# Kernel tuning notes

Hardware: AMD Instinct MI355X
Metric: run time of the kernel (lower is better)

## Reference

```python
import jax, jax.numpy as jnp
import numpy as np

N = 50000
E_RAND = 800000
F_IN = 128
HID = 128
HEADS = 8
LAYERS = 2
DH = HID // HEADS  # 16


def setup_inputs() -> dict:
    key = jax.random.key(0)
    ks = jax.random.split(key, 8)
    x = jax.random.normal(ks[0], (N, F_IN), dtype=jnp.float32)
    # random edges + self loops so every row of the segment-softmax is nonempty
    rnd = jax.random.randint(ks[1], (2, E_RAND), 0, N, dtype=jnp.int32)
    loops = jnp.tile(jnp.arange(N, dtype=jnp.int32), (2, 1))
    edge_idx = jnp.concatenate([rnd, loops], axis=1)  # [2, 850000]
    edge_vals = jnp.ones((edge_idx.shape[1],), dtype=jnp.float32)
    # glorot-style params
    enc_W = jax.random.normal(ks[2], (F_IN, HID), dtype=jnp.float32) * np.sqrt(2.0 / (F_IN + HID))
    enc_b = jnp.zeros((HID,), dtype=jnp.float32)
    W_stack = jax.random.normal(ks[3], (LAYERS, HEADS, HID, DH), dtype=jnp.float32) * np.sqrt(2.0 / (HID + DH))
    a_stack = jax.random.normal(ks[4], (LAYERS, HEADS, 2 * DH), dtype=jnp.float32) * np.sqrt(2.0 / (1 + 2 * DH))
    return {"x": x, "edge_idx": edge_idx, "edge_vals": edge_vals,
            "enc_W": enc_W, "enc_b": enc_b, "W_stack": W_stack, "a_stack": a_stack}


def _gat_layer(xin, row, col, edge_vals, W, a):
    # xin: [N, HID]; W: [H, HID, DH]; a: [H, 2*DH]
    n = xin.shape[0]
    h = jnp.einsum('nd,hdf->hnf', xin, W)            # [H, N, DH]
    a_src, a_dst = a[:, :DH], a[:, DH:]
    alpha_src = jnp.einsum('hnf,hf->hn', h, a_src)   # a . h[row] part
    alpha_dst = jnp.einsum('hnf,hf->hn', h, a_dst)   # a . h[col] part
    logits = edge_vals[None, :] * (alpha_src[:, row] + alpha_dst[:, col])  # [H, E]
    e = jnp.exp(jax.nn.leaky_relu(logits, 0.2))      # unnormalized attention
    rowsum = jax.ops.segment_sum(e.T, row, num_segments=n)               # [N, H]
    msg = e[:, :, None] * h[:, col, :]               # [H, E, DH]
    agg = jax.vmap(lambda m: jax.ops.segment_sum(m, row, num_segments=n))(msg)  # [H, N, DH]
    out = agg / rowsum.T[:, :, None]
    return jnp.transpose(out, (1, 0, 2)).reshape(n, -1)  # concat heads -> [N, HID]


def reference(x, edge_idx, edge_vals, enc_W, enc_b, W_stack, a_stack):
    row, col = edge_idx[0], edge_idx[1]
    xc = x @ enc_W + enc_b  # encoder
    L = W_stack.shape[0]
    for ell in range(L):
        out = _gat_layer(xc, row, col, edge_vals, W_stack[ell], a_stack[ell])
        if ell != L - 1:
            out = jax.nn.elu(out)  # feat_drop is identity in eval mode
        xc = out + xc if ell > 0 else out  # use_residual=True
    # single snapshot: stack over T=1 then permute(1,0,2) -> [N, 1, HID]
    return xc[:, None, :]
```

## Files before the change

kernel.cpp:

```cpp
#include <hip/hip_runtime.h>
#include <hip/hip_bf16.h>


typedef __attribute__((ext_vector_type(8))) short short8;
typedef __attribute__((ext_vector_type(4))) float floatx4;
typedef __attribute__((ext_vector_type(2))) float floatx2;

__device__ __forceinline__ unsigned f2u(float f) { return __float_as_uint(f); }
__device__ __forceinline__ float u2f(unsigned u) { return __uint_as_float(u); }
__device__ __forceinline__ unsigned short f2bf_rne(float x) {
    unsigned u = f2u(x);
    unsigned r = (u + 0x7FFF + ((u >> 16) & 1)) >> 16;
    return (unsigned short)r;
}
__device__ __forceinline__ float bf2f(unsigned short b) { return u2f(((unsigned)b) << 16); }


__global__ void histpack_kernel(const int* __restrict__ row, int* __restrict__ deg,
                                int* __restrict__ rank, int E, int EB,
                                const float* __restrict__ encW,
                                const float* __restrict__ Wstack,
                                short8* __restrict__ Wh, short8* __restrict__ Wl) {
    int b = blockIdx.x;
    if (b < EB) {
        int e = b * 256 + threadIdx.x;
        if (e < E) rank[e] = atomicAdd(&deg[row[e]], 1);
        return;
    }
    int idx = (b - EB) * 256 + threadIdx.x;
    if (idx >= 3 * 2048) return;
    int mat = idx >> 11;
    int r = idx & 2047;
    int lane = r & 63;
    int tile = r >> 6;
    int ct = tile >> 2, kt = tile & 3;
    int ncol = ct * 16 + (lane & 15);
    int k0 = kt * 32 + ((lane >> 4) * 8);
    short8 hv, lv;
#pragma unroll
    for (int j = 0; j < 8; ++j) {
        int k = k0 + j;
        float w = (mat == 0)
            ? encW[k * 128 + ncol]
            : Wstack[(mat - 1) * 16384 + (ncol >> 4) * 2048 + k * 16 + (ncol & 15)];
        unsigned u = f2u(w);
        hv[j] = (short)(u >> 16);
        float hf = u2f(u & 0xFFFF0000u);
        float l = w - hf;
        lv[j] = (short)(f2u(l) >> 16);
    }
    Wh[idx] = hv;
    Wl[idx] = lv;
}

__global__ void scan_atomic_kernel(const int* __restrict__ deg, int* __restrict__ rowstart,
                                   int* __restrict__ gcursor, int n) {
    __shared__ int sd[512];
    __shared__ int sbase;
    int t = threadIdx.x;
    int idx = blockIdx.x * 512 + t;
    int v = (idx < n) ? deg[idx] : 0;
    sd[t] = v;
    __syncthreads();
    for (int off = 1; off < 512; off <<= 1) {
        int add = (t >= off) ? sd[t - off] : 0;
        __syncthreads();
        sd[t] += add;
        __syncthreads();
    }
    if (t == 511) sbase = atomicAdd(gcursor, sd[511]);
    __syncthreads();
    if (idx < n) rowstart[idx] = sbase + sd[t] - v;
}

__global__ void scatterperm_kernel(const int* __restrict__ row, const int* __restrict__ rank,
                                   const int* __restrict__ rowstart, int* __restrict__ perm,
                                   int E) {
    int e = blockIdx.x * 256 + threadIdx.x;
    if (e < E) perm[rowstart[row[e]] + rank[e]] = e;
}

__global__ void gathercv_kernel(const int* __restrict__ perm, const int* __restrict__ colv,
                                const float* __restrict__ ev, int2* __restrict__ csr_cv,
                                int E) {
    int s = blockIdx.x * 256 + threadIdx.x;
    if (s < E) {
        int e = perm[s];
        csr_cv[s] = make_int2(colv[e], __float_as_int(ev[e]));
    }
}


__global__ __launch_bounds__(256) void
gemm_mfma(const float* __restrict__ A, const short8* __restrict__ Bh,
          const short8* __restrict__ Bl, const float* __restrict__ bias,
          const float* __restrict__ avec, float* __restrict__ Cf,
          unsigned short* __restrict__ Cbf,
          float* __restrict__ asrc, float* __restrict__ adst, int n, int flags) {
    int wave = threadIdx.x >> 6;
    int lane = threadIdx.x & 63;
    int q = lane >> 4;
    int col = lane & 15;
    int n0w = blockIdx.x * 64 + wave * 16;

    int arow = min(n0w + col, n - 1);
    const float* Arow = A + (size_t)arow * 128;
    int kb = q * 8;
    short8 Ah[4], Al[4];
#pragma unroll
    for (int kt = 0; kt < 4; ++kt) {
        float4 f0 = *(const float4*)(Arow + kt * 32 + kb);
        float4 f1 = *(const float4*)(Arow + kt * 32 + kb + 4);
        float fv[8] = {f0.x, f0.y, f0.z, f0.w, f1.x, f1.y, f1.z, f1.w};
#pragma unroll
        for (int j = 0; j < 8; ++j) {
            unsigned u = f2u(fv[j]);
            Ah[kt][j] = (short)(u >> 16);
            float hf = u2f(u & 0xFFFF0000u);
            float l = fv[j] - hf;
            Al[kt][j] = (short)(f2u(l) >> 16);
        }
    }

    int nbase = n0w + q * 4;
#pragma unroll
    for (int ct = 0; ct < 8; ++ct) {
        short8 bh[4], bl[4];
#pragma unroll
        for (int kt = 0; kt < 4; ++kt) {
            bh[kt] = Bh[(ct * 4 + kt) * 64 + lane];
            bl[kt] = Bl[(ct * 4 + kt) * 64 + lane];
        }
        float bv = (flags & 1) ? bias[ct * 16 + col] : 0.f;
        floatx4 acc = {bv, bv, bv, bv};
#pragma unroll
        for (int kt = 0; kt < 4; ++kt) {
            acc = __builtin_amdgcn_mfma_f32_16x16x32_bf16(Ah[kt], bh[kt], acc, 0, 0, 0);
            acc = __builtin_amdgcn_mfma_f32_16x16x32_bf16(Al[kt], bh[kt], acc, 0, 0, 0);
            acc = __builtin_amdgcn_mfma_f32_16x16x32_bf16(Ah[kt], bl[kt], acc, 0, 0, 0);
        }
#pragma unroll
        for (int reg = 0; reg < 4; ++reg) {
            int node = nbase + reg;
            if (node < n) {
                if (flags & 4) Cbf[(size_t)node * 128 + ct * 16 + col] = f2bf_rne(acc[reg]);
                else           Cf[(size_t)node * 128 + ct * 16 + col] = acc[reg];
            }
        }
        if (flags & 2) {
            float a_s = avec[ct * 32 + col];
            float a_d = avec[ct * 32 + 16 + col];
#pragma unroll
            for (int reg = 0; reg < 4; ++reg) {
                float ps = acc[reg] * a_s;
                float pd = acc[reg] * a_d;
#pragma unroll
                for (int off = 8; off; off >>= 1) {
                    ps += __shfl_down(ps, off, 16);
                    pd += __shfl_down(pd, off, 16);
                }
                int node = nbase + reg;
                if (col == 0 && node < n) {
                    asrc[node * 8 + ct] = ps;
                    adst[node * 8 + ct] = pd;
                }
            }
        }
    }
}


#define PROC(W, JJ) if ((JJ) < e) {                                        \
    int c = (W).x;                                                          \
    float v = __int_as_float((W).y);                                        \
    float lg = v * (as_w + adst[c * 8 + h]);                                \
    float lr = fmaxf(lg, 0.2f * lg);                                        \
    float w = __expf(lr);                                                   \
    uint4 hv = *(const uint4*)(hbf + (size_t)c * 128 + l4 * 8);             \
    floatx2 wv = {w, w};                                                    \
    floatx2 p0 = {u2f(hv.x << 16), u2f(hv.x & 0xFFFF0000u)};                \
    floatx2 p1 = {u2f(hv.y << 16), u2f(hv.y & 0xFFFF0000u)};                \
    floatx2 p2 = {u2f(hv.z << 16), u2f(hv.z & 0xFFFF0000u)};                \
    floatx2 p3 = {u2f(hv.w << 16), u2f(hv.w & 0xFFFF0000u)};                \
    acc0 += wv * p0; acc1 += wv * p1; acc2 += wv * p2; acc3 += wv * p3;     \
    ws += w; }

__global__ __launch_bounds__(256) void
aggregate_kernel(const int* __restrict__ rowstart, const int* __restrict__ degv,
                 const int2* __restrict__ cv,
                 const unsigned short* __restrict__ hbf,
                 const float* __restrict__ asrc, const float* __restrict__ adst,
                 const float* __restrict__ resid, float* __restrict__ out,
                 int mode, int n) {
    int wid = (blockIdx.x * 256 + threadIdx.x) >> 6;
    if (wid >= n) return;
    int lane = threadIdx.x & 63;
    int grp = lane >> 4;
    int l4 = lane & 15;
    int h = l4 >> 1;

    int s = rowstart[wid];
    int e = s + degv[wid];
    float as_w = asrc[wid * 8 + h];

    floatx2 acc0 = {0.f, 0.f}, acc1 = {0.f, 0.f};
    floatx2 acc2 = {0.f, 0.f}, acc3 = {0.f, 0.f};
    float ws = 0.f;

    int jb = s + grp;
    int2 s0 = {0, 0}, s1 = {0, 0}, s2 = {0, 0}, s3 = {0, 0};
    if (jb      < e) s0 = cv[jb];
    if (jb + 4  < e) s1 = cv[jb + 4];
    if (jb + 8  < e) s2 = cv[jb + 8];
    if (jb + 12 < e) s3 = cv[jb + 12];

    while (jb < e) {
        int2 e0 = s0, e1 = s1, e2 = s2, e3 = s3;
        int jn = jb + 16;
        if (jn      < e) s0 = cv[jn];
        if (jn + 4  < e) s1 = cv[jn + 4];
        if (jn + 8  < e) s2 = cv[jn + 8];
        if (jn + 12 < e) s3 = cv[jn + 12];
        PROC(e0, jb)
        PROC(e1, jb + 4)
        PROC(e2, jb + 8)
        PROC(e3, jb + 12)
        jb = jn;
    }

    float a0 = acc0.x, a1 = acc0.y, a2 = acc1.x, a3 = acc1.y;
    float a4 = acc2.x, a5 = acc2.y, a6 = acc3.x, a7 = acc3.y;

#define RED4(x) x += __shfl_xor(x, 16); x += __shfl_xor(x, 32);
    RED4(a0) RED4(a1) RED4(a2) RED4(a3)
    RED4(a4) RED4(a5) RED4(a6) RED4(a7)
    RED4(ws)
#undef RED4

    if (grp == 0) {
        float inv = 1.0f / ws;
        float o[8] = {a0 * inv, a1 * inv, a2 * inv, a3 * inv,
                      a4 * inv, a5 * inv, a6 * inv, a7 * inv};
        size_t base = (size_t)wid * 128 + l4 * 8;
        if (mode == 0) {
#pragma unroll
            for (int k = 0; k < 8; ++k) o[k] = o[k] > 0.f ? o[k] : expm1f(o[k]);
        } else {
            float4 r0 = *(const float4*)(resid + base);
            float4 r1 = *(const float4*)(resid + base + 4);
            o[0] += r0.x; o[1] += r0.y; o[2] += r0.z; o[3] += r0.w;
            o[4] += r1.x; o[5] += r1.y; o[6] += r1.z; o[7] += r1.w;
        }
        float4 w0 = {o[0], o[1], o[2], o[3]};
        float4 w1 = {o[4], o[5], o[6], o[7]};
        *(float4*)(out + base) = w0;
        *(float4*)(out + base + 4) = w1;
    }
}
#undef PROC


extern "C" void kernel_launch(void* const* d_in, const int* in_sizes, int n_in,
                              void* d_out, int out_size, void* d_ws, size_t ws_size,
                              hipStream_t stream) {
    const int N = in_sizes[0] / 128;
    const int E = in_sizes[2];

    const float* x      = (const float*)d_in[0];
    const int*   eidx   = (const int*)d_in[1];
    const float* ev     = (const float*)d_in[2];
    const float* encW   = (const float*)d_in[3];
    const float* encb   = (const float*)d_in[4];
    const float* Wstack = (const float*)d_in[5];
    const float* astack = (const float*)d_in[6];
    float* out = (float*)d_out;

    const int* row = eidx;
    const int* colv = eidx + E;

    char* p = (char*)d_ws;
    float* xc   = (float*)p; p += (size_t)N * 128 * 4;
    float* xcB  = (float*)p; p += (size_t)N * 128 * 4;
    unsigned short* hbf = (unsigned short*)p; p += (size_t)N * 128 * 2;
    float* asrc = (float*)p; p += (size_t)N * 8 * 4;
    float* adst = (float*)p; p += (size_t)N * 8 * 4;
    short8* Wh  = (short8*)p; p += 3 * 2048 * 16;
    short8* Wl  = (short8*)p; p += 3 * 2048 * 16;
    int2* csr_cv = (int2*)p; p += (size_t)E * 8;
    int* rowstart = (int*)p; p += (size_t)N * 4;
    int* deg    = (int*)p;   p += (size_t)N * 4;
    int* gcursor = (int*)p;  p += 4;

    int* rank = (int*)xc;
    int* perm = rank + E;

    const int NB = (N + 511) / 512;
    const int GB = (N + 63) / 64;
    const int AGG = (N + 3) / 4;
    const int EB = (E + 255) / 256;

    hipMemsetAsync(deg, 0, (size_t)(N + 1) * 4, stream);
    histpack_kernel<<<EB + 24, 256, 0, stream>>>(row, deg, rank, E, EB,
                                                 encW, Wstack, Wh, Wl);
    scan_atomic_kernel<<<NB, 512, 0, stream>>>(deg, rowstart, gcursor, N);
    scatterperm_kernel<<<EB, 256, 0, stream>>>(row, rank, rowstart, perm, E);
    gathercv_kernel<<<EB, 256, 0, stream>>>(perm, colv, ev, csr_cv, E);

    gemm_mfma<<<GB, 256, 0, stream>>>(x, Wh, Wl, encb, nullptr, xc, nullptr,
                                      nullptr, nullptr, N, 1);

    gemm_mfma<<<GB, 256, 0, stream>>>(xc, Wh + 2048, Wl + 2048, nullptr, astack,
                                      nullptr, hbf, asrc, adst, N, 2 | 4);
    aggregate_kernel<<<AGG, 256, 0, stream>>>(rowstart, deg, csr_cv, hbf, asrc, adst,
                                              nullptr, xcB, 0, N);

    gemm_mfma<<<GB, 256, 0, stream>>>(xcB, Wh + 4096, Wl + 4096, nullptr, astack + 256,
                                      nullptr, hbf, asrc, adst, N, 2 | 4);
    aggregate_kernel<<<AGG, 256, 0, stream>>>(rowstart, deg, csr_cv, hbf, asrc, adst,
                                              xcB, out, 1, N);
}
```

Baseline: 317.4 us.

## Fuse encoder GEMM with degree scan and layer-1 GEMM with edge scatter

Merges independent work into shared launches. The encoder GEMM blocks and the row-offset scan blocks now run in one grid, and the layer-1 projection GEMM runs alongside the CSR permutation scatter. The rank/perm scratch moves from xc to xcB so the buffers do not collide. This cuts two kernel launches and lets the preprocessing overlap with the GEMMs. The aggregate loop's manual prefetch pipeline is also replaced by a simple unrolled loop, which may lower memory-level parallelism.

```diff
diff --git a/kernel.cpp b/kernel.cpp
--- a/kernel.cpp
+++ b/kernel.cpp
@@ -13,7 +13,6 @@
     unsigned r = (u + 0x7FFF + ((u >> 16) & 1)) >> 16;
     return (unsigned short)r;
 }
-__device__ __forceinline__ float bf2f(unsigned short b) { return u2f(((unsigned)b) << 16); }
 
 
 __global__ void histpack_kernel(const int* __restrict__ row, int* __restrict__ deg,
@@ -53,33 +52,6 @@
     Wl[idx] = lv;
 }
 
-__global__ void scan_atomic_kernel(const int* __restrict__ deg, int* __restrict__ rowstart,
-                                   int* __restrict__ gcursor, int n) {
-    __shared__ int sd[512];
-    __shared__ int sbase;
-    int t = threadIdx.x;
-    int idx = blockIdx.x * 512 + t;
-    int v = (idx < n) ? deg[idx] : 0;
-    sd[t] = v;
-    __syncthreads();
-    for (int off = 1; off < 512; off <<= 1) {
-        int add = (t >= off) ? sd[t - off] : 0;
-        __syncthreads();
-        sd[t] += add;
-        __syncthreads();
-    }
-    if (t == 511) sbase = atomicAdd(gcursor, sd[511]);
-    __syncthreads();
-    if (idx < n) rowstart[idx] = sbase + sd[t] - v;
-}
-
-__global__ void scatterperm_kernel(const int* __restrict__ row, const int* __restrict__ rank,
-                                   const int* __restrict__ rowstart, int* __restrict__ perm,
-                                   int E) {
-    int e = blockIdx.x * 256 + threadIdx.x;
-    if (e < E) perm[rowstart[row[e]] + rank[e]] = e;
-}
-
 __global__ void gathercv_kernel(const int* __restrict__ perm, const int* __restrict__ colv,
                                 const float* __restrict__ ev, int2* __restrict__ csr_cv,
                                 int E) {
@@ -91,8 +63,8 @@
 }
 
 
-__global__ __launch_bounds__(256) void
-gemm_mfma(const float* __restrict__ A, const short8* __restrict__ Bh,
+__device__ __forceinline__ void
+gemm_body(int bid, const float* __restrict__ A, const short8* __restrict__ Bh,
           const short8* __restrict__ Bl, const float* __restrict__ bias,
           const float* __restrict__ avec, float* __restrict__ Cf,
           unsigned short* __restrict__ Cbf,
@@ -101,7 +73,7 @@
     int lane = threadIdx.x & 63;
     int q = lane >> 4;
     int col = lane & 15;
-    int n0w = blockIdx.x * 64 + wave * 16;
+    int n0w = bid * 64 + wave * 16;
 
     int arow = min(n0w + col, n - 1);
     const float* Arow = A + (size_t)arow * 128;
@@ -169,21 +141,57 @@
     }
 }
 
-
-#define PROC(W, JJ) if ((JJ) < e) {                                        \
-    int c = (W).x;                                                          \
-    float v = __int_as_float((W).y);                                        \
-    float lg = v * (as_w + adst[c * 8 + h]);                                \
-    float lr = fmaxf(lg, 0.2f * lg);                                        \
-    float w = __expf(lr);                                                   \
-    uint4 hv = *(const uint4*)(hbf + (size_t)c * 128 + l4 * 8);             \
-    floatx2 wv = {w, w};                                                    \
-    floatx2 p0 = {u2f(hv.x << 16), u2f(hv.x & 0xFFFF0000u)};                \
-    floatx2 p1 = {u2f(hv.y << 16), u2f(hv.y & 0xFFFF0000u)};                \
-    floatx2 p2 = {u2f(hv.z << 16), u2f(hv.z & 0xFFFF0000u)};                \
-    floatx2 p3 = {u2f(hv.w << 16), u2f(hv.w & 0xFFFF0000u)};                \
-    acc0 += wv * p0; acc1 += wv * p1; acc2 += wv * p2; acc3 += wv * p3;     \
-    ws += w; }
+__global__ __launch_bounds__(256) void
+gemm_mfma(const float* __restrict__ A, const short8* __restrict__ Bh,
+          const short8* __restrict__ Bl, const float* __restrict__ avec,
+          unsigned short* __restrict__ Cbf,
+          float* __restrict__ asrc, float* __restrict__ adst, int n) {
+    gemm_body(blockIdx.x, A, Bh, Bl, nullptr, avec, nullptr, Cbf, asrc, adst, n, 2 | 4);
+}
+
+__global__ __launch_bounds__(256) void
+enc_scan_kernel(const float* __restrict__ x, const short8* __restrict__ Wh,
+                const short8* __restrict__ Wl, const float* __restrict__ encb,
+                float* __restrict__ xc, int n, int GBn,
+                const int* __restrict__ deg, int* __restrict__ rowstart,
+                int* __restrict__ gcursor) {
+    __shared__ int sd[256];
+    __shared__ int sbase;
+    if ((int)blockIdx.x < GBn) {
+        gemm_body(blockIdx.x, x, Wh, Wl, encb, nullptr, xc, nullptr, nullptr, nullptr, n, 1);
+        return;
+    }
+    int t = threadIdx.x;
+    int idx = (blockIdx.x - GBn) * 256 + t;
+    int v = (idx < n) ? deg[idx] : 0;
+    sd[t] = v;
+    __syncthreads();
+    for (int off = 1; off < 256; off <<= 1) {
+        int add = (t >= off) ? sd[t - off] : 0;
+        __syncthreads();
+        sd[t] += add;
+        __syncthreads();
+    }
+    if (t == 255) sbase = atomicAdd(gcursor, sd[255]);
+    __syncthreads();
+    if (idx < n) rowstart[idx] = sbase + sd[t] - v;
+}
+
+__global__ __launch_bounds__(256) void
+sperm_gemm_kernel(const float* __restrict__ xc, const short8* __restrict__ Wh1,
+                  const short8* __restrict__ Wl1, const float* __restrict__ avec,
+                  unsigned short* __restrict__ hbf, float* __restrict__ asrc,
+                  float* __restrict__ adst, int n, int GBn,
+                  const int* __restrict__ row, const int* __restrict__ rank,
+                  const int* __restrict__ rowstart, int* __restrict__ perm, int E) {
+    if ((int)blockIdx.x < GBn) {
+        gemm_body(blockIdx.x, xc, Wh1, Wl1, nullptr, avec, nullptr, hbf, asrc, adst, n, 2 | 4);
+        return;
+    }
+    int e = (blockIdx.x - GBn) * 256 + threadIdx.x;
+    if (e < E) perm[rowstart[row[e]] + rank[e]] = e;
+}
+
 
 __global__ __launch_bounds__(256) void
 aggregate_kernel(const int* __restrict__ rowstart, const int* __restrict__ degv,
@@ -207,25 +215,25 @@
     floatx2 acc2 = {0.f, 0.f}, acc3 = {0.f, 0.f};
     float ws = 0.f;
 
-    int jb = s + grp;
-    int2 s0 = {0, 0}, s1 = {0, 0}, s2 = {0, 0}, s3 = {0, 0};
-    if (jb      < e) s0 = cv[jb];
-    if (jb + 4  < e) s1 = cv[jb + 4];
-    if (jb + 8  < e) s2 = cv[jb + 8];
-    if (jb + 12 < e) s3 = cv[jb + 12];
-
-    while (jb < e) {
-        int2 e0 = s0, e1 = s1, e2 = s2, e3 = s3;
-        int jn = jb + 16;
-        if (jn      < e) s0 = cv[jn];
-        if (jn + 4  < e) s1 = cv[jn + 4];
-        if (jn + 8  < e) s2 = cv[jn + 8];
-        if (jn + 12 < e) s3 = cv[jn + 12];
-        PROC(e0, jb)
-        PROC(e1, jb + 4)
-        PROC(e2, jb + 8)
-        PROC(e3, jb + 12)
-        jb = jn;
+#pragma unroll 4
+    for (int j = s + grp; j < e; j += 4) {
+        int2 cvj = cv[j];
+        int c = cvj.x;
+        float v = __int_as_float(cvj.y);
+        float lg = v * (as_w + adst[c * 8 + h]);
+        float lr = fmaxf(lg, 0.2f * lg);
+        float w = __expf(lr);
+        uint4 hv = *(const uint4*)(hbf + (size_t)c * 128 + l4 * 8);
+        floatx2 w2 = {w, w};
+        floatx2 p0 = {u2f(hv.x << 16), u2f(hv.x & 0xFFFF0000u)};
+        floatx2 p1 = {u2f(hv.y << 16), u2f(hv.y & 0xFFFF0000u)};
+        floatx2 p2 = {u2f(hv.z << 16), u2f(hv.z & 0xFFFF0000u)};
+        floatx2 p3 = {u2f(hv.w << 16), u2f(hv.w & 0xFFFF0000u)};
+        acc0 += w2 * p0;
+        acc1 += w2 * p1;
+        acc2 += w2 * p2;
+        acc3 += w2 * p3;
+        ws += w;
     }
 
     float a0 = acc0.x, a1 = acc0.y, a2 = acc1.x, a3 = acc1.y;
@@ -257,7 +265,6 @@
         *(float4*)(out + base + 4) = w1;
     }
 }
-#undef PROC
 
 
 extern "C" void kernel_launch(void* const* d_in, const int* in_sizes, int n_in,
@@ -291,10 +298,10 @@
     int* deg    = (int*)p;   p += (size_t)N * 4;
     int* gcursor = (int*)p;  p += 4;
 
-    int* rank = (int*)xc;
+    int* rank = (int*)xcB;
     int* perm = rank + E;
 
-    const int NB = (N + 511) / 512;
+    const int NB256 = (N + 255) / 256;
     const int GB = (N + 63) / 64;
     const int AGG = (N + 3) / 4;
     const int EB = (E + 255) / 256;
@@ -302,20 +309,21 @@
     hipMemsetAsync(deg, 0, (size_t)(N + 1) * 4, stream);
     histpack_kernel<<<EB + 24, 256, 0, stream>>>(row, deg, rank, E, EB,
                                                  encW, Wstack, Wh, Wl);
-    scan_atomic_kernel<<<NB, 512, 0, stream>>>(deg, rowstart, gcursor, N);
-    scatterperm_kernel<<<EB, 256, 0, stream>>>(row, rank, rowstart, perm, E);
+
+    enc_scan_kernel<<<GB + NB256, 256, 0, stream>>>(x, Wh, Wl, encb, xc, N, GB,
+                                                    deg, rowstart, gcursor);
+
+    sperm_gemm_kernel<<<GB + EB, 256, 0, stream>>>(xc, Wh + 2048, Wl + 2048, astack,
+                                                   hbf, asrc, adst, N, GB,
+                                                   row, rank, rowstart, perm, E);
+
     gathercv_kernel<<<EB, 256, 0, stream>>>(perm, colv, ev, csr_cv, E);
 
-    gemm_mfma<<<GB, 256, 0, stream>>>(x, Wh, Wl, encb, nullptr, xc, nullptr,
-                                      nullptr, nullptr, N, 1);
-
-    gemm_mfma<<<GB, 256, 0, stream>>>(xc, Wh + 2048, Wl + 2048, nullptr, astack,
-                                      nullptr, hbf, asrc, adst, N, 2 | 4);
     aggregate_kernel<<<AGG, 256, 0, stream>>>(rowstart, deg, csr_cv, hbf, asrc, adst,
                                               nullptr, xcB, 0, N);
 
-    gemm_mfma<<<GB, 256, 0, stream>>>(xcB, Wh + 4096, Wl + 4096, nullptr, astack + 256,
-                                      nullptr, hbf, asrc, adst, N, 2 | 4);
+    gemm_mfma<<<GB, 256, 0, stream>>>(xcB, Wh + 4096, Wl + 4096, astack + 256,
+                                      hbf, asrc, adst, N);
     aggregate_kernel<<<AGG, 256, 0, stream>>>(rowstart, deg, csr_cv, hbf, asrc, adst,
                                               xcB, out, 1, N);
 }
```

New measurement: 301.7 us. 1.05x faster.
